# Kernel tuning notes

Hardware: AMD Instinct MI355X
Metric: run time of the kernel (lower is better)

Reference implementation:

```python
import jax, jax.numpy as jnp
import numpy as np

NUM_HEADS = 8


def setup_inputs() -> dict:
    key = jax.random.key(0)
    ks = jax.random.split(key, 8)
    B, N, H, W = 8, 1024, 32, 32
    dim = H * W  # 1024
    x1 = jax.random.normal(ks[0], (B, N, H, W), dtype=jnp.float32)
    x2 = jax.random.normal(ks[1], (B, N, H, W), dtype=jnp.float32)
    conv_w = jax.random.normal(ks[2], (N, 2 * N, 3, 3), dtype=jnp.float32) * 0.01
    conv_b = jnp.zeros((N,), dtype=jnp.float32)
    wq = jax.random.normal(ks[3], (dim, dim), dtype=jnp.float32) * 0.02
    wk = jax.random.normal(ks[4], (dim, dim), dtype=jnp.float32) * 0.02
    wv = jax.random.normal(ks[5], (dim, dim), dtype=jnp.float32) * 0.02
    proj_w = jax.random.normal(ks[6], (dim, dim), dtype=jnp.float32) * 0.02
    proj_b = jnp.zeros((dim,), dtype=jnp.float32)
    return {"x1": x1, "x2": x2, "conv_w": conv_w, "conv_b": conv_b,
            "wq": wq, "wk": wk, "wv": wv, "proj_w": proj_w, "proj_b": proj_b}


def reference(x1, x2, conv_w, conv_b, wq, wk, wv, proj_w, proj_b):
    B, N, H, W = x1.shape
    C = H * W
    nh = NUM_HEADS
    hd = C // nh
    scale = hd ** -0.5

    # conv_cat: Conv2d(2N -> N, k=3, pad=1) on channel-concatenated inputs
    x_cat = jnp.concatenate([x1, x2], axis=1)  # [B, 2N, H, W]
    x_cat = jax.lax.conv_general_dilated(
        x_cat, conv_w, window_strides=(1, 1), padding=((1, 1), (1, 1)),
        dimension_numbers=("NCHW", "OIHW", "NCHW"))
    x_cat = x_cat + conv_b[None, :, None, None]
    x_cat = x_cat.reshape(B, N, C)  # [B, N, C]

    # torch Linear: y = x @ W.T (no bias, qkv_bias=False)
    def heads(t):  # [B, N, C] -> [B, nh, N, hd]
        return t.reshape(B, N, nh, hd).transpose(0, 2, 1, 3)

    q = heads(x1.reshape(B, N, C) @ wq.T)
    k = heads(x_cat @ wk.T)
    v = heads(x_cat @ wv.T)

    # attention: softmax(q k^T * scale) v   (dropout is identity at p=0)
    attn = jnp.einsum("bhnd,bhmd->bhnm", q, k) * scale
    attn = jax.nn.softmax(attn, axis=-1)
    x_attn = jnp.einsum("bhnm,bhmd->bhnd", attn, v)  # [B, nh, N, hd]
    x_attn = x_attn.transpose(0, 2, 1, 3).reshape(B, N, C)

    out = (x_attn @ proj_w.T + proj_b).reshape(B, N, H, W) + x1
    return out
```

## Files before the change

### kernel.cpp

```cpp
#include <hip/hip_runtime.h>
#include <hip/hip_bf16.h>
#include <cstdint>
#include <cstddef>

typedef __attribute__((ext_vector_type(8))) short short8;
typedef __attribute__((ext_vector_type(4))) float f32x4;
typedef unsigned short u16;

static __device__ __forceinline__ u16 f2bf(float f) {
  __hip_bfloat16 h = __float2bfloat16(f);
  return *reinterpret_cast<u16*>(&h);
}

static __device__ __forceinline__ void gload16(const void* g, void* l) {
  __builtin_amdgcn_global_load_lds(
      (const __attribute__((address_space(1))) void*)g,
      (__attribute__((address_space(3))) void*)l, 16, 0, 0);
}


__global__ void cast4_k(const float* __restrict__ a, const float* __restrict__ b,
                        const float* __restrict__ c, const float* __restrict__ d,
                        u16* __restrict__ oa, u16* __restrict__ ob,
                        u16* __restrict__ oc, u16* __restrict__ od) {
  const int which = blockIdx.y;
  const float* src = (which == 0) ? a : (which == 1) ? b : (which == 2) ? c : d;
  u16* dst = (which == 0) ? oa : (which == 1) ? ob : (which == 2) ? oc : od;
  int i = blockIdx.x * 256 + threadIdx.x;
  float4 v = ((const float4*)src)[i];
  union { u16 u[4]; uint2 p; } r;
  r.u[0] = f2bf(v.x); r.u[1] = f2bf(v.y); r.u[2] = f2bf(v.z); r.u[3] = f2bf(v.w);
  ((uint2*)dst)[i] = r.p;
}

__global__ void build_pad(const float* __restrict__ x1, const float* __restrict__ x2,
                          u16* __restrict__ in_t_pad, u16* __restrict__ x1b) {
  __shared__ float tile[64][65];
  const int it = blockIdx.x;
  const int st = blockIdx.y;
  const int b  = blockIdx.z;
  const int i0 = it * 64, s0 = st * 64;
  const bool isx1 = (i0 < 1024);
  const float* src = isx1
      ? x1 + ((size_t)b * 1024 + i0) * 1024
      : x2 + ((size_t)b * 1024 + (i0 - 1024)) * 1024;
  const int t = threadIdx.x;
  #pragma unroll
  for (int jj = 0; jj < 16; ++jj) {
    int idx = jj * 256 + t;
    int ii = idx >> 6, si = idx & 63;
    float v = src[(size_t)ii * 1024 + s0 + si];
    tile[ii][si] = v;
    if (isx1)
      x1b[((size_t)b * 1024 + i0 + ii) * 1024 + s0 + si] = f2bf(v);
  }
  __syncthreads();
  #pragma unroll
  for (int jj = 0; jj < 16; ++jj) {
    int idx = jj * 256 + t;
    int si = idx >> 6, ii = idx & 63;
    const int s = s0 + si;
    const int prow = (b * 34 + (s >> 5) + 1) * 34 + (s & 31) + 1;
    in_t_pad[(size_t)prow * 2048 + i0 + ii] = f2bf(tile[ii][si]);
  }
}

__global__ void pack_wp(const float* __restrict__ cw, u16* __restrict__ Wp) {
  __shared__ float sb[2304];
  const int blk = blockIdx.x;
  const int t = threadIdx.x;
  const size_t base = (size_t)blk * 2304;
  #pragma unroll
  for (int jj = 0; jj < 9; ++jj) sb[jj * 256 + t] = cw[base + jj * 256 + t];
  __syncthreads();
  const int p = blk * 256 + t;
  #pragma unroll
  for (int q = 0; q < 9; ++q)
    Wp[(size_t)q * 2097152 + p] = f2bf(sb[t * 9 + q]);
}

__global__ void addc_k(const float* __restrict__ p, const float* __restrict__ bias,
                       u16* __restrict__ xc) {
  __shared__ float tile[64][65];
  const int st = blockIdx.x;
  const int ot = blockIdx.y;
  const int b  = blockIdx.z;
  const int s0 = st * 64, o0 = ot * 64;
  const int t = threadIdx.x;
  const float* p1 = p + 8388608;
  #pragma unroll
  for (int jj = 0; jj < 16; ++jj) {
    int idx = jj * 256 + t;
    int si = idx >> 6, oi = idx & 63;
    const size_t m = ((size_t)b * 1024 + s0 + si) * 1024 + o0 + oi;
    tile[si][oi] = p[m] + p1[m] + bias[o0 + oi];
  }
  __syncthreads();
  #pragma unroll
  for (int jj = 0; jj < 16; ++jj) {
    int idx = jj * 256 + t;
    int oi = idx >> 6, si = idx & 63;
    xc[((size_t)b * 1024 + o0 + oi) * 1024 + s0 + si] = f2bf(tile[si][oi]);
  }
}

enum { GM_PLAIN = 0, GM_PROJ = 2, GM_KV = 4 };

__global__ __launch_bounds__(256, 1)
void conv9_k(const u16* __restrict__ Ap, const u16* __restrict__ B,
             float* __restrict__ Cf) {
  __shared__ u16 lds[2 * 12288 + 3 * 8192];
  const int tid = threadIdx.x;
  const int lane = tid & 63, w = tid >> 6;
  const int l15 = lane & 15, l4 = lane >> 4;

  const int bid = blockIdx.x;
  const int lb = (bid & 7) * 32 + (bid >> 3);
  const int kz = lb >> 7;
  const int tile = lb & 127;
  const int tm = tile >> 2, tn = tile & 3;
  const int row0 = tm * 256, col0 = tn * 256;
  const int b = tm >> 2;
  const int y0 = (tm & 3) * 8;
  const int hb = (b * 34 + y0) * 34;
  const int wr = (w >> 1) * 128, wc = (w & 1) * 128;
  const int chbase = kz * 1024;

  int pr[8];
  #pragma unroll
  for (int mi = 0; mi < 8; ++mi) {
    const int m = row0 + wr + mi * 16 + l15;
    const int y = (m >> 5) & 31, x = m & 31;
    pr[mi] = (y - y0 + 1) * 34 + x + 1;
  }

  const int srow = tid >> 2;
  const int sgc = tid & 3;

  f32x4 acc[8][8];
  #pragma unroll
  for (int i = 0; i < 8; ++i)
    #pragma unroll
    for (int jj = 0; jj < 8; ++jj)
      acc[i][jj] = (f32x4){0.f, 0.f, 0.f, 0.f};

  auto stageHalo = [&](int cc, int half) {
    u16* dst = lds + half * 12288;
    #pragma unroll
    for (int rnd = 0; rnd < 6; ++rnd) {
      const int row = rnd * 64 + srow;
      const int g = sgc ^ ((row >> 1) & 3);
      const u16* src = Ap + (size_t)(hb + row) * 2048 + chbase + cc * 32 + g * 8;
      gload16(src, dst + (size_t)(rnd * 256 + tid) * 8);
    }
  };
  auto stageB = [&](int cc, int q) {
    u16* dst = lds + 24576 + (q % 3) * 8192;
    #pragma unroll
    for (int rnd = 0; rnd < 4; ++rnd) {
      const int r = rnd * 64 + srow;
      const int g = sgc ^ ((r >> 1) & 3);
      const u16* src = B + ((size_t)q << 21) + (size_t)(col0 + r) * 2048
                       + chbase + cc * 32 + g * 8;
      gload16(src, dst + (size_t)(rnd * 256 + tid) * 8);
    }
  };

  constexpr int ddt[9] = {-35, -34, -33, -1, 0, 1, 33, 34, 35};
  constexpr int NC = 32;

  stageHalo(0, 0);
  stageHalo(1, 1);
  stageB(0, 0);
  stageB(0, 1);

  for (int cc = 0; cc < NC; ++cc) {
    const u16* hcur = lds + (cc & 1) * 12288;
    const bool interior = (cc >= 1 && cc <= NC - 2);
    #pragma unroll
    for (int q = 0; q < 9; ++q) {
      if ((q == 1 || q == 2) && interior) {
        asm volatile("s_waitcnt vmcnt(10)" ::: "memory");
      } else if (q == 8 && cc == NC - 1) {
        asm volatile("s_waitcnt vmcnt(0)" ::: "memory");
      } else {
        asm volatile("s_waitcnt vmcnt(4)" ::: "memory");
      }
      __builtin_amdgcn_s_barrier();
      {
        const int gp2 = cc * 9 + q + 2;
        if (gp2 <= NC * 9 - 1) {
          int qS = q + 2, ccS = cc;
          if (qS >= 9) { qS -= 9; ccS += 1; }
          stageB(ccS, qS);
        }
        if (q == 0 && cc >= 1 && cc <= NC - 2)
          stageHalo(cc + 1, (cc + 1) & 1);
      }
      {
        const u16* bq = lds + 24576 + (q % 3) * 8192;
        const int dd = ddt[q];
        short8 av[8], bv[8];
        #pragma unroll
        for (int mi = 0; mi < 8; ++mi) {
          const int hr = pr[mi] + dd;
          const int g = l4 ^ ((hr >> 1) & 3);
          av[mi] = *(const short8*)(hcur + hr * 32 + g * 8);
        }
        #pragma unroll
        for (int ni = 0; ni < 8; ++ni) {
          const int r = wc + ni * 16 + l15;
          const int g = l4 ^ ((r >> 1) & 3);
          bv[ni] = *(const short8*)(bq + r * 32 + g * 8);
        }
        __builtin_amdgcn_s_setprio(1);
        #pragma unroll
        for (int mi = 0; mi < 8; ++mi)
          #pragma unroll
          for (int ni = 0; ni < 8; ++ni)
            acc[mi][ni] = __builtin_amdgcn_mfma_f32_16x16x32_bf16(av[mi], bv[ni], acc[mi][ni], 0, 0, 0);
        __builtin_amdgcn_s_setprio(0);
      }
    }
  }

  #pragma unroll
  for (int mi = 0; mi < 8; ++mi) {
    #pragma unroll
    for (int ni = 0; ni < 8; ++ni) {
      #pragma unroll
      for (int j = 0; j < 4; ++j) {
        const int grow = row0 + wr + mi * 16 + l4 * 4 + j;
        const int gcol = col0 + wc + ni * 16 + l15;
        Cf[(size_t)kz * 8388608 + ((size_t)grow << 10) + gcol] = acc[mi][ni][j];
      }
    }
  }
}

template<int MODE>
__global__ __launch_bounds__(512, 2)
void gemm3_k(const u16* __restrict__ A, const u16* __restrict__ B,
             u16* __restrict__ Cb, float* __restrict__ Cf,
             const float* __restrict__ bias, const float* __restrict__ resid,
             int Ktot, int ntn_sh) {
  __shared__ u16 lds[3 * 24576];
  const int tid = threadIdx.x;
  const int lane = tid & 63;
  const int w = tid >> 6;
  const int l15 = lane & 15, l4 = lane >> 4;

  const int nwg = gridDim.x;
  const int bid = blockIdx.x;
  const int lb = (bid & 7) * (nwg >> 3) + (bid >> 3);
  const int tm = lb >> ntn_sh;
  const int tn = lb & ((1 << ntn_sh) - 1);
  const int row0 = tm * 256, col0 = tn * 128;
  const int wr = (w >> 1) * 64, wc = (w & 1) * 64;

  const int sr = w * 8 + (lane >> 3);
  const int pp = (lane & 7) ^ (lane >> 3);

  f32x4 acc[4][4];
  #pragma unroll
  for (int i = 0; i < 4; ++i)
    #pragma unroll
    for (int jj = 0; jj < 4; ++jj)
      acc[i][jj] = (f32x4){0.f, 0.f, 0.f, 0.f};

  const int nK = Ktot >> 6;

  auto stage = [&](int kt, u16* buf) {
    u16* da = buf + (size_t)w * 512;
    u16* db = buf + 16384 + (size_t)w * 512;
    const int k0 = kt << 6;
    #pragma unroll
    for (int u = 0; u < 4; ++u) {
      const u16* ga = A + (size_t)(row0 + u * 64 + sr) * Ktot + k0 + pp * 8;
      gload16(ga, da + u * 4096);
    }
    #pragma unroll
    for (int u = 0; u < 2; ++u) {
      const u16* gb = B + (size_t)(col0 + u * 64 + sr) * Ktot + k0 + pp * 8;
      gload16(gb, db + u * 4096);
    }
  };

  auto compute = [&](const u16* buf) {
    const char* Ar = (const char*)buf;
    const char* Br = (const char*)(buf + 16384);
    #pragma unroll
    for (int ks = 0; ks < 2; ++ks) {
      const int bcol = ((ks << 6) + (l4 << 4)) ^ ((l15 & 7) << 4);
      short8 av[4], bv[4];
      #pragma unroll
      for (int mi = 0; mi < 4; ++mi)
        av[mi] = *(const short8*)(Ar + (wr + mi * 16 + l15) * 128 + bcol);
      #pragma unroll
      for (int ni = 0; ni < 4; ++ni)
        bv[ni] = *(const short8*)(Br + (wc + ni * 16 + l15) * 128 + bcol);
      __builtin_amdgcn_s_setprio(1);
      #pragma unroll
      for (int mi = 0; mi < 4; ++mi)
        #pragma unroll
        for (int ni = 0; ni < 4; ++ni)
          acc[mi][ni] = __builtin_amdgcn_mfma_f32_16x16x32_bf16(av[mi], bv[ni], acc[mi][ni], 0, 0, 0);
      __builtin_amdgcn_s_setprio(0);
    }
  };

  u16* pb0 = lds;
  u16* pb1 = lds + 24576;
  u16* pb2 = lds + 49152;

  stage(0, pb0);
  stage(1, pb1);
  for (int t = 0; t < nK; ++t) {
    if (t + 1 < nK) {
      asm volatile("s_waitcnt vmcnt(6)" ::: "memory");
    } else {
      asm volatile("s_waitcnt vmcnt(0)" ::: "memory");
    }
    __builtin_amdgcn_s_barrier();
    if (t + 2 < nK) stage(t + 2, pb2);
    compute(pb0);
    u16* tmp = pb0; pb0 = pb1; pb1 = pb2; pb2 = tmp;
  }

  #pragma unroll
  for (int mi = 0; mi < 4; ++mi) {
    #pragma unroll
    for (int ni = 0; ni < 4; ++ni) {
      #pragma unroll
      for (int j = 0; j < 4; ++j) {
        const int grow = row0 + wr + mi * 16 + l4 * 4 + j;
        const int gcol = col0 + wc + ni * 16 + l15;
        const float v = acc[mi][ni][j];
        if constexpr (MODE == GM_PLAIN) {
          Cb[((size_t)grow << 10) + gcol] = f2bf(v);
        } else if constexpr (MODE == GM_PROJ) {
          const size_t o = ((size_t)grow << 10) + gcol;
          Cf[o] = v + bias[gcol] + resid[o];
        }
      }
    }
  }
}

template<int MODE>
__global__ __launch_bounds__(512, 4)
void gemm5_k(const u16* __restrict__ A, const u16* __restrict__ B,
             u16* __restrict__ Cb, u16* __restrict__ Cb2,
             int Ktot, int ntn_sh) {
  __shared__ u16 lds[3 * 12288];
  const int tid = threadIdx.x;
  const int lane = tid & 63;
  const int w = tid >> 6;
  const int l15 = lane & 15, l4 = lane >> 4;

  const int nwg = gridDim.x;
  const int bid = blockIdx.x;
  const int lb = (bid & 7) * (nwg >> 3) + (bid >> 3);
  const int tm = lb >> ntn_sh;
  const int tn = lb & ((1 << ntn_sh) - 1);
  const int row0 = tm * 256, col0 = tn * 128;
  const int wr = (w >> 1) * 64, wc = (w & 1) * 64;

  const int str = tid >> 2;
  const int sgc = tid & 3;

  f32x4 acc[4][4];
  #pragma unroll
  for (int i = 0; i < 4; ++i)
    #pragma unroll
    for (int jj = 0; jj < 4; ++jj)
      acc[i][jj] = (f32x4){0.f, 0.f, 0.f, 0.f};

  const int nKt = Ktot >> 5;

  auto stage = [&](int kt, u16* buf) {
    const int k0 = kt << 5;
    #pragma unroll
    for (int u = 0; u < 2; ++u) {
      const int r = u * 128 + str;
      const int swz = sgc ^ ((r >> 1) & 3);
      const u16* ga = A + (size_t)(row0 + r) * Ktot + k0 + swz * 8;
      gload16(ga, buf + ((size_t)u * 512 + tid) * 8);
    }
    {
      const int swz = sgc ^ ((str >> 1) & 3);
      const u16* gb = B + (size_t)(col0 + str) * Ktot + k0 + swz * 8;
      gload16(gb, buf + 8192 + (size_t)tid * 8);
    }
  };

  auto compute = [&](const u16* buf) {
    short8 av[4], bv[4];
    #pragma unroll
    for (int mi = 0; mi < 4; ++mi) {
      const int row = wr + mi * 16 + l15;
      const int g = l4 ^ ((row >> 1) & 3);
      av[mi] = *(const short8*)(buf + row * 32 + g * 8);
    }
    #pragma unroll
    for (int ni = 0; ni < 4; ++ni) {
      const int row = wc + ni * 16 + l15;
      const int g = l4 ^ ((row >> 1) & 3);
      bv[ni] = *(const short8*)(buf + 8192 + row * 32 + g * 8);
    }
    __builtin_amdgcn_s_setprio(1);
    #pragma unroll
    for (int mi = 0; mi < 4; ++mi)
      #pragma unroll
      for (int ni = 0; ni < 4; ++ni)
        acc[mi][ni] = __builtin_amdgcn_mfma_f32_16x16x32_bf16(av[mi], bv[ni], acc[mi][ni], 0, 0, 0);
    __builtin_amdgcn_s_setprio(0);
  };

  u16* pb0 = lds;
  u16* pb1 = lds + 12288;
  u16* pb2 = lds + 24576;

  stage(0, pb0);
  stage(1, pb1);
  for (int t = 0; t < nKt; ++t) {
    if (t + 1 < nKt) {
      asm volatile("s_waitcnt vmcnt(3)" ::: "memory");
    } else {
      asm volatile("s_waitcnt vmcnt(0)" ::: "memory");
    }
    __builtin_amdgcn_s_barrier();
    if (t + 2 < nKt) stage(t + 2, pb2);
    compute(pb0);
    u16* tmp = pb0; pb0 = pb1; pb1 = pb2; pb2 = tmp;
  }

  #pragma unroll
  for (int mi = 0; mi < 4; ++mi) {
    #pragma unroll
    for (int ni = 0; ni < 4; ++ni) {
      #pragma unroll
      for (int j = 0; j < 4; ++j) {
        const int grow = row0 + wr + mi * 16 + l4 * 4 + j;
        const int gcol = col0 + wc + ni * 16 + l15;
        const float v = acc[mi][ni][j];
        if constexpr (MODE == GM_KV) {
          if (gcol < 1024) {
            Cb[((size_t)grow << 10) + gcol] = f2bf(v);
          } else {
            const int c = gcol - 1024;
            const int b = grow >> 10, ms = grow & 1023;
            const int h = c >> 7, d = c & 127;
            Cb2[((size_t)((b * 8 + h) * 128 + d) << 10) + ms] = f2bf(v);
          }
        }
      }
    }
  }
}

__global__ __launch_bounds__(256, 2)
void attn2_k(const u16* __restrict__ Q, const u16* __restrict__ K,
             const u16* __restrict__ Vt, u16* __restrict__ O) {
  __shared__ u16 Ks[2][64 * 128];
  __shared__ u16 Vs[2][128 * 64];
  __shared__ u16 Plds[4][16 * 80];
  const int bid = blockIdx.x;
  const int lb = (bid & 7) * 128 + (bid >> 3);
  const int bh = lb >> 4;
  const int mtile = lb & 15;
  const int b = bh >> 3, h = bh & 7;
  const int tid = threadIdx.x, lane = tid & 63, w = tid >> 6;
  const int l15 = lane & 15, l4 = lane >> 4;

  short8 qf[4];
  {
    const int qrow = b * 1024 + mtile * 64 + w * 16 + l15;
    const u16* qb = Q + ((size_t)qrow << 10) + h * 128;
    #pragma unroll
    for (int kk = 0; kk < 4; ++kk)
      qf[kk] = *(const short8*)(qb + kk * 32 + l4 * 8);
  }

  f32x4 o[8];
  #pragma unroll
  for (int db = 0; db < 8; ++db) o[db] = (f32x4){0.f, 0.f, 0.f, 0.f};
  float mrow[4], lrow[4];
  #pragma unroll
  for (int j = 0; j < 4; ++j) { mrow[j] = -1e30f; lrow[j] = 0.f; }
  const float scale = 0.08838834764831845f;

  auto stageKV = [&](int kt, int half) {
    #pragma unroll
    for (int j = 0; j < 4; ++j) {
      const int c = (j * 4 + w) * 64 + lane;
      const int r = c >> 4;
      const int coff = (((c & 15) ^ (r & 7)) << 3);
      const u16* gp = K + ((size_t)(b * 1024 + kt * 64 + r) << 10) + h * 128 + coff;
      gload16(gp, (void*)(Ks[half] + (j * 4 + w) * 512));
    }
    #pragma unroll
    for (int j = 0; j < 4; ++j) {
      const int c = (j * 4 + w) * 64 + lane;
      const int r = c >> 3;
      const int coff = (((c & 7) ^ (r & 7)) << 3);
      const u16* gp = Vt + ((size_t)((b * 8 + h) * 128 + r) << 10) + kt * 64 + coff;
      gload16(gp, (void*)(Vs[half] + (j * 4 + w) * 512));
    }
  };

  stageKV(0, 0);
  for (int kt = 0; kt < 16; ++kt) {
    const int cur = kt & 1;
    asm volatile("s_waitcnt vmcnt(0)" ::: "memory");
    __builtin_amdgcn_s_barrier();
    if (kt + 1 < 16) stageKV(kt + 1, cur ^ 1);

    const u16* ks_ = Ks[cur];
    const u16* vs_ = Vs[cur];
    f32x4 s[4];
    #pragma unroll
    for (int cb = 0; cb < 4; ++cb) {
      s[cb] = (f32x4){0.f, 0.f, 0.f, 0.f};
      #pragma unroll
      for (int kk = 0; kk < 4; ++kk) {
        const int col = (kk * 32 + l4 * 8) ^ ((l15 & 7) << 3);
        short8 bK = *(const short8*)(ks_ + (cb * 16 + l15) * 128 + col);
        s[cb] = __builtin_amdgcn_mfma_f32_16x16x32_bf16(qf[kk], bK, s[cb], 0, 0, 0);
      }
    }
    #pragma unroll
    for (int cb = 0; cb < 4; ++cb) {
      s[cb][0] *= scale; s[cb][1] *= scale; s[cb][2] *= scale; s[cb][3] *= scale;
    }
    #pragma unroll
    for (int j = 0; j < 4; ++j) {
      float mx = fmaxf(fmaxf(s[0][j], s[1][j]), fmaxf(s[2][j], s[3][j]));
      #pragma unroll
      for (int off = 8; off >= 1; off >>= 1)
        mx = fmaxf(mx, __shfl_xor(mx, off, 64));
      const float mn = fmaxf(mrow[j], mx);
      const float fac = __expf(mrow[j] - mn);
      mrow[j] = mn;
      float rs = 0.f;
      #pragma unroll
      for (int cb = 0; cb < 4; ++cb) {
        const float p = __expf(s[cb][j] - mn);
        s[cb][j] = p;
        rs += p;
      }
      #pragma unroll
      for (int off = 8; off >= 1; off >>= 1)
        rs += __shfl_xor(rs, off, 64);
      lrow[j] = lrow[j] * fac + rs;
      #pragma unroll
      for (int db = 0; db < 8; ++db) o[db][j] *= fac;
    }
    u16* pl = Plds[w];
    #pragma unroll
    for (int cb = 0; cb < 4; ++cb)
      #pragma unroll
      for (int j = 0; j < 4; ++j)
        pl[(l4 * 4 + j) * 80 + cb * 16 + l15] = f2bf(s[cb][j]);
    asm volatile("s_waitcnt lgkmcnt(0)" ::: "memory");
    __builtin_amdgcn_sched_barrier(0);
    short8 ap[2];
    #pragma unroll
    for (int ks2 = 0; ks2 < 2; ++ks2)
      ap[ks2] = *(const short8*)(pl + l15 * 80 + ks2 * 32 + l4 * 8);
    #pragma unroll
    for (int db = 0; db < 8; ++db) {
      #pragma unroll
      for (int ks2 = 0; ks2 < 2; ++ks2) {
        const int col = (ks2 * 32 + l4 * 8) ^ ((l15 & 7) << 3);
        short8 bV = *(const short8*)(vs_ + (db * 16 + l15) * 64 + col);
        o[db] = __builtin_amdgcn_mfma_f32_16x16x32_bf16(ap[ks2], bV, o[db], 0, 0, 0);
      }
    }
  }
  #pragma unroll
  for (int db = 0; db < 8; ++db) {
    #pragma unroll
    for (int j = 0; j < 4; ++j) {
      const int grow = b * 1024 + mtile * 64 + w * 16 + l4 * 4 + j;
      const int gcol = h * 128 + db * 16 + l15;
      O[((size_t)grow << 10) + gcol] = f2bf(o[db][j] / lrow[j]);
    }
  }
}


extern "C" void kernel_launch(void* const* d_in, const int* in_sizes, int n_in,
                              void* d_out, int out_size, void* d_ws, size_t ws_size,
                              hipStream_t stream) {
  const float* x1     = (const float*)d_in[0];
  const float* x2     = (const float*)d_in[1];
  const float* conv_w = (const float*)d_in[2];
  const float* conv_b = (const float*)d_in[3];
  const float* wq     = (const float*)d_in[4];
  const float* wk     = (const float*)d_in[5];
  const float* wv     = (const float*)d_in[6];
  const float* proj_w = (const float*)d_in[7];
  const float* proj_b = (const float*)d_in[8];
  float* out = (float*)d_out;

  char* ws = (char*)d_ws;
  size_t off = 0;
  auto alloc = [&](size_t bytes) -> void* {
    void* p = ws + off;
    off += (bytes + 255) & ~(size_t)255;
    return p;
  };
  u16* x1b  = (u16*)alloc(8192ULL * 1024 * 2);
  u16* in_t_pad = (u16*)alloc((9248ULL + 96) * 2048 * 2);
  const size_t pad_bytes = 9248ULL * 2048 * 2;
  u16* Wp   = (u16*)alloc(9ULL * 2097152 * 2);
  u16* wqb  = (u16*)alloc(1048576ULL * 2);
  u16* wkb  = (u16*)alloc(1048576ULL * 2);
  u16* wvb  = (u16*)alloc(1048576ULL * 2);
  u16* pjb  = (u16*)alloc(1048576ULL * 2);
  u16* xc   = (u16*)alloc(8192ULL * 1024 * 2);
  u16* Qb   = (u16*)alloc(8192ULL * 1024 * 2);
  u16* Kb   = (u16*)alloc(8192ULL * 1024 * 2);
  u16* Vtb  = (u16*)alloc(8192ULL * 1024 * 2);
  u16* Ob   = (u16*)alloc(8192ULL * 1024 * 2);
  float* pConv = (float*)Qb;

  (void)hipMemsetAsync(in_t_pad, 0, pad_bytes + 96ULL * 2048 * 2, stream);
  cast4_k<<<dim3(1024, 4), 256, 0, stream>>>(wq, wk, wv, proj_w, wqb, wkb, wvb, pjb);
  build_pad<<<dim3(32, 16, 8), 256, 0, stream>>>(x1, x2, in_t_pad, x1b);
  pack_wp<<<8192, 256, 0, stream>>>(conv_w, Wp);

  conv9_k<<<256, 256, 0, stream>>>(in_t_pad, Wp, pConv);
  addc_k<<<dim3(16, 16, 8), 256, 0, stream>>>(pConv, conv_b, xc);
  gemm3_k<GM_PLAIN><<<256, 512, 0, stream>>>(x1b, wqb, Qb, nullptr, nullptr, nullptr, 1024, 3);
  gemm5_k<GM_KV><<<512, 512, 0, stream>>>(xc, wkb, Kb, Vtb, 1024, 4);
  attn2_k<<<1024, 256, 0, stream>>>(Qb, Kb, Vtb, Ob);
  gemm3_k<GM_PROJ><<<256, 512, 0, stream>>>(Ob, pjb, nullptr, out, proj_b, x1, 1024, 3);
}
```

Baseline: 519.8 us.

## Load conv weight fragments directly into registers instead of staging through LDS

The conv kernel stops staging the per-tap weight tiles through a triple-buffered LDS ring and has each wave load its B fragments straight from global memory into registers, prefetching one tap ahead. This cuts the per-tap barriers down to one barrier per channel chunk and shrinks LDS use. The cost is more global or L2 traffic, because the two waves sharing a column half now each load the same weights. It also adds register pressure from the three register buffers, and a full vmcnt(0) wait per chunk that serialises the halo and weight loads.

Result: slower. 690.1 us (+32.8%).

```diff
diff --git a/kernel.cpp b/kernel.cpp
--- a/kernel.cpp
+++ b/kernel.cpp
@@ -107,9 +107,9 @@
 enum { GM_PLAIN = 0, GM_PROJ = 2, GM_KV = 4 };
 
 __global__ __launch_bounds__(256, 1)
-void conv9_k(const u16* __restrict__ Ap, const u16* __restrict__ B,
-             float* __restrict__ Cf) {
-  __shared__ u16 lds[2 * 12288 + 3 * 8192];
+void conv10_k(const u16* __restrict__ Ap, const u16* __restrict__ B,
+              float* __restrict__ Cf) {
+  __shared__ u16 lds[2 * 12288];
   const int tid = threadIdx.x;
   const int lane = tid & 63, w = tid >> 6;
   const int l15 = lane & 15, l4 = lane >> 4;
@@ -154,16 +154,13 @@
       gload16(src, dst + (size_t)(rnd * 256 + tid) * 8);
     }
   };
-  auto stageB = [&](int cc, int q) {
-    u16* dst = lds + 24576 + (q % 3) * 8192;
-    #pragma unroll
-    for (int rnd = 0; rnd < 4; ++rnd) {
-      const int r = rnd * 64 + srow;
-      const int g = sgc ^ ((r >> 1) & 3);
-      const u16* src = B + ((size_t)q << 21) + (size_t)(col0 + r) * 2048
-                       + chbase + cc * 32 + g * 8;
-      gload16(src, dst + (size_t)(rnd * 256 + tid) * 8);
-    }
+
+  short8 bvr[3][8];
+  auto loadB = [&](int cc, int q, int buf) {
+    const u16* bp = B + ((size_t)q << 21) + chbase + cc * 32 + l4 * 8;
+    #pragma unroll
+    for (int ni = 0; ni < 8; ++ni)
+      bvr[buf][ni] = *(const short8*)(bp + (size_t)(col0 + wc + ni * 16 + l15) * 2048);
   };
 
   constexpr int ddt[9] = {-35, -34, -33, -1, 0, 1, 33, 34, 35};
@@ -171,56 +168,36 @@
 
   stageHalo(0, 0);
   stageHalo(1, 1);
-  stageB(0, 0);
-  stageB(0, 1);
+  loadB(0, 0, 0);
 
   for (int cc = 0; cc < NC; ++cc) {
+    asm volatile("s_waitcnt vmcnt(0)" ::: "memory");
+    __builtin_amdgcn_s_barrier();
+    if (cc >= 1 && cc <= NC - 2)
+      stageHalo(cc + 1, (cc + 1) & 1);
     const u16* hcur = lds + (cc & 1) * 12288;
-    const bool interior = (cc >= 1 && cc <= NC - 2);
     #pragma unroll
     for (int q = 0; q < 9; ++q) {
-      if ((q == 1 || q == 2) && interior) {
-        asm volatile("s_waitcnt vmcnt(10)" ::: "memory");
-      } else if (q == 8 && cc == NC - 1) {
-        asm volatile("s_waitcnt vmcnt(0)" ::: "memory");
-      } else {
-        asm volatile("s_waitcnt vmcnt(4)" ::: "memory");
-      }
-      __builtin_amdgcn_s_barrier();
-      {
-        const int gp2 = cc * 9 + q + 2;
-        if (gp2 <= NC * 9 - 1) {
-          int qS = q + 2, ccS = cc;
-          if (qS >= 9) { qS -= 9; ccS += 1; }
-          stageB(ccS, qS);
-        }
-        if (q == 0 && cc >= 1 && cc <= NC - 2)
-          stageHalo(cc + 1, (cc + 1) & 1);
-      }
-      {
-        const u16* bq = lds + 24576 + (q % 3) * 8192;
-        const int dd = ddt[q];
-        short8 av[8], bv[8];
+      if (q < 8) {
+        loadB(cc, q + 1, (q + 1) % 3);
+      } else if (cc + 1 < NC) {
+        loadB(cc + 1, 0, 0);
+      }
+      const int dd = ddt[q];
+      short8 av[8];
+      #pragma unroll
+      for (int mi = 0; mi < 8; ++mi) {
+        const int hr = pr[mi] + dd;
+        const int g = l4 ^ ((hr >> 1) & 3);
+        av[mi] = *(const short8*)(hcur + hr * 32 + g * 8);
+      }
+      __builtin_amdgcn_s_setprio(1);
+      #pragma unroll
+      for (int mi = 0; mi < 8; ++mi)
         #pragma unroll
-        for (int mi = 0; mi < 8; ++mi) {
-          const int hr = pr[mi] + dd;
-          const int g = l4 ^ ((hr >> 1) & 3);
-          av[mi] = *(const short8*)(hcur + hr * 32 + g * 8);
-        }
-        #pragma unroll
-        for (int ni = 0; ni < 8; ++ni) {
-          const int r = wc + ni * 16 + l15;
-          const int g = l4 ^ ((r >> 1) & 3);
-          bv[ni] = *(const short8*)(bq + r * 32 + g * 8);
-        }
-        __builtin_amdgcn_s_setprio(1);
-        #pragma unroll
-        for (int mi = 0; mi < 8; ++mi)
-          #pragma unroll
-          for (int ni = 0; ni < 8; ++ni)
-            acc[mi][ni] = __builtin_amdgcn_mfma_f32_16x16x32_bf16(av[mi], bv[ni], acc[mi][ni], 0, 0, 0);
-        __builtin_amdgcn_s_setprio(0);
-      }
+        for (int ni = 0; ni < 8; ++ni)
+          acc[mi][ni] = __builtin_amdgcn_mfma_f32_16x16x32_bf16(av[mi], bvr[q % 3][ni], acc[mi][ni], 0, 0, 0);
+      __builtin_amdgcn_s_setprio(0);
     }
   }
 
@@ -631,7 +608,7 @@
   build_pad<<<dim3(32, 16, 8), 256, 0, stream>>>(x1, x2, in_t_pad, x1b);
   pack_wp<<<8192, 256, 0, stream>>>(conv_w, Wp);
 
-  conv9_k<<<256, 256, 0, stream>>>(in_t_pad, Wp, pConv);
+  conv10_k<<<256, 256, 0, stream>>>(in_t_pad, Wp, pConv);
   addc_k<<<dim3(16, 16, 8), 256, 0, stream>>>(pConv, conv_b, xc);
   gemm3_k<GM_PLAIN><<<256, 512, 0, stream>>>(x1b, wqb, Qb, nullptr, nullptr, nullptr, 1024, 3);
   gemm5_k<GM_KV><<<512, 512, 0, stream>>>(xc, wkb, Kb, Vtb, 1024, 4);
```
